# Optimization experiments

Hardware: AMD Instinct MI355X
Metric: run time of the kernel (lower is better)

The kernel has to match this reference:

```python
import jax, jax.numpy as jnp
import numpy as np

N = 100000   # nodes
E = 600000   # edges
D = 128      # in_dim == out_dim
ED = 6       # edge_dim
LN_EPS = 1e-5


def setup_inputs() -> dict:
    key = jax.random.key(0)
    ks = jax.random.split(key, 12)
    s = 1.0 / np.sqrt(D)
    se = 1.0 / np.sqrt(ED)
    return {
        "x": jax.random.normal(ks[0], (N, D), dtype=jnp.float32),
        "edge_index": jax.random.randint(ks[1], (2, E), 0, N, dtype=jnp.int64),
        "edge_attr": jax.random.normal(ks[2], (E, ED), dtype=jnp.float32),
        "batch": jnp.zeros((N,), dtype=jnp.int64),
        "W_e": jax.random.uniform(ks[3], (ED, D), jnp.float32, -se, se),
        "b_e": jax.random.uniform(ks[4], (D,), jnp.float32, -se, se),
        "eps": jnp.zeros((), dtype=jnp.float32),  # GINE train_eps init 0
        "W1": jax.random.uniform(ks[5], (D, D), jnp.float32, -s, s),
        "b1": jax.random.uniform(ks[6], (D,), jnp.float32, -s, s),
        "W2": jax.random.uniform(ks[7], (D, D), jnp.float32, -s, s),
        "b2": jax.random.uniform(ks[8], (D,), jnp.float32, -s, s),
        "gamma": jnp.ones((D,), dtype=jnp.float32),
        "beta": jnp.zeros((D,), dtype=jnp.float32),
    }


def reference(x, edge_index, edge_attr, batch, W_e, b_e, eps, W1, b1, W2, b2, gamma, beta):
    src, dst = edge_index[0], edge_index[1]
    # edge embedding: Linear(edge_dim -> in_dim)
    edge_emb = edge_attr @ W_e + b_e                      # [E, D]
    # GINEConv message: ReLU(x_j + edge_emb), scatter-add to target nodes
    msg = jax.nn.relu(x[src] + edge_emb)                  # [E, D]
    agg = jax.ops.segment_sum(msg, dst, num_segments=N)   # [N, D]
    h = (1.0 + eps) * x + agg                             # [N, D]
    # GINE nn: Linear -> ReLU -> Linear
    h = jax.nn.relu(h @ W1 + b1) @ W2 + b2                # [N, D]
    # LayerNorm over feature dim
    mu = jnp.mean(h, axis=-1, keepdims=True)
    var = jnp.var(h, axis=-1, keepdims=True)
    h = (h - mu) * jax.lax.rsqrt(var + LN_EPS) * gamma + beta
    # activation=True -> ReLU; dropout identity in eval mode
    return jax.nn.relu(h)
```

## Files before the change

### kernel.cpp

```cpp
#include <hip/hip_runtime.h>
#include <stdint.h>

#define NN 100000
#define EE 600000
#define DD 128

typedef _Float16 half8 __attribute__((ext_vector_type(8)));
typedef _Float16 h2 __attribute__((ext_vector_type(2)));
typedef float f32x4 __attribute__((ext_vector_type(4)));

static __device__ __forceinline__ uint32_t pack2(float a, float b) {
    h2 h; h.x = (_Float16)a; h.y = (_Float16)b;
    return __builtin_bit_cast(uint32_t, h);
}
static __device__ __forceinline__ h2 cvt22(float2 f) {
    h2 r; r.x = (_Float16)f.x; r.y = (_Float16)f.y; return r;
}
static __device__ __forceinline__ h2 bc_lo(h2 v) { h2 r; r.x = v.x; r.y = v.x; return r; }
static __device__ __forceinline__ h2 bc_hi(h2 v) { h2 r; r.x = v.y; r.y = v.y; return r; }

static __device__ __forceinline__ uint32_t edge_msg2(uint32_t rY, uint32_t rZ, uint32_t rW,
                                                     uint32_t xv, uint32_t bb,
                                                     uint32_t w0, uint32_t w1, uint32_t w2,
                                                     uint32_t w3, uint32_t w4, uint32_t w5)
{
    uint32_t m;
    asm("v_pk_fma_f16 %0, %1, %2, %3 op_sel:[0,0,0] op_sel_hi:[0,1,1]"
        : "=v"(m) : "v"(rY), "v"(w0), "v"(bb));
    asm("v_pk_fma_f16 %0, %1, %2, %0 op_sel:[1,0,0] op_sel_hi:[1,1,1]" : "+v"(m) : "v"(rY), "v"(w1));
    asm("v_pk_fma_f16 %0, %1, %2, %0 op_sel:[0,0,0] op_sel_hi:[0,1,1]" : "+v"(m) : "v"(rZ), "v"(w2));
    asm("v_pk_fma_f16 %0, %1, %2, %0 op_sel:[1,0,0] op_sel_hi:[1,1,1]" : "+v"(m) : "v"(rZ), "v"(w3));
    asm("v_pk_fma_f16 %0, %1, %2, %0 op_sel:[0,0,0] op_sel_hi:[0,1,1]" : "+v"(m) : "v"(rW), "v"(w4));
    asm("v_pk_fma_f16 %0, %1, %2, %0 op_sel:[1,0,0] op_sel_hi:[1,1,1]" : "+v"(m) : "v"(rW), "v"(w5));
    asm("v_pk_add_f16 %0, %0, %1" : "+v"(m) : "v"(xv));
    asm("v_pk_max_f16 %0, %0, 0" : "+v"(m));
    return m;
}

#define NB_HIST ((EE + 255) / 256)
#define NB_CONV (NN * DD / 4 / 256)
template<bool CONV>
__global__ __launch_bounds__(256)
void setup_kernel(const int* __restrict__ ei, const float* __restrict__ x,
                  const float* __restrict__ W1, const float* __restrict__ W2,
                  int* __restrict__ counts, uint32_t* __restrict__ xh,
                  _Float16* __restrict__ w1h, _Float16* __restrict__ w2h)
{
    const int nbc = CONV ? NB_CONV : 0;
    const int b = blockIdx.x, tid = threadIdx.x;
    if (b < NB_HIST) {
        int e = b * 256 + tid;
        if (e < EE) atomicAdd(&counts[ei[EE + e]], 1);
    } else if (CONV && b < NB_HIST + nbc) {
        int i = (b - NB_HIST) * 256 + tid;
        float4 v = ((const float4*)x)[i];
        uint2 o; o.x = pack2(v.x, v.y); o.y = pack2(v.z, v.w);
        ((uint2*)xh)[i] = o;
    } else {
        int t = (b - NB_HIST - nbc) * 256 + tid;
        if (t < 2 * DD * DD) {
            int which = t >> 14;
            int idx = t & (DD * DD - 1);
            int k = idx >> 7, d = idx & 127;
            float wv = (which ? W2 : W1)[k * DD + d];
            int kt = k >> 5, kr = k & 31;
            int grp = kr >> 3, j = kr & 7;
            int nt = d >> 4, cc = d & 15;
            int off = ((kt * 8 + nt) * 64 + grp * 16 + cc) * 8 + j;
            (which ? w2h : w1h)[off] = (_Float16)wv;
        }
    }
}

__global__ __launch_bounds__(256)
void scan_blocks(const int* __restrict__ counts, int* __restrict__ startv,
                 int* __restrict__ bsum)
{
    const int t = threadIdx.x;
    const int idx = blockIdx.x * 1024 + t * 4;
    int4 v = {0, 0, 0, 0};
    if (idx < NN) v = *(const int4*)(counts + idx);
    int s1 = v.x + v.y, s2 = s1 + v.z, s3 = s2 + v.w;
    const int lane = t & 63;
    int q = s3;
#pragma unroll
    for (int off = 1; off < 64; off <<= 1) {
        int u = __shfl_up(q, off, 64);
        if (lane >= off) q += u;
    }
    __shared__ int wsum[4];
    if (lane == 63) wsum[t >> 6] = q;
    __syncthreads();
    const int w = t >> 6;
    int pre = 0;
    if (w > 0) pre += wsum[0];
    if (w > 1) pre += wsum[1];
    if (w > 2) pre += wsum[2];
    const int excl = (q - s3) + pre;
    if (idx < NN) {
        int4 o = {excl, excl + v.x, excl + s1, excl + s2};
        *(int4*)(startv + idx) = o;
    }
    __syncthreads();
    if (t == 0) bsum[blockIdx.x] = wsum[0] + wsum[1] + wsum[2] + wsum[3];
}

__global__ __launch_bounds__(128)
void scan_top(const int* __restrict__ bsum, int* __restrict__ boff)
{
    __shared__ int sm[128];
    const int t = threadIdx.x;
    const int NB = (NN + 1023) / 1024;
    int v = (t < NB) ? bsum[t] : 0;
    sm[t] = v;
    __syncthreads();
#pragma unroll
    for (int off = 1; off < 128; off <<= 1) {
        int u = (t >= off) ? sm[t - off] : 0;
        __syncthreads();
        sm[t] += u;
        __syncthreads();
    }
    boff[t] = sm[t] - v;
}

__global__ __launch_bounds__(256)
void scatter_rec(const int* __restrict__ ei, const float* __restrict__ ea,
                 const int* __restrict__ start, const int* __restrict__ boff,
                 int* __restrict__ cursor, float* __restrict__ rec)
{
    int e = blockIdx.x * 256 + threadIdx.x;
    if (e >= EE) return;
    int dst = ei[EE + e];
    int src = ei[e];
    int pos = start[dst] + boff[dst >> 10] + atomicAdd(&cursor[dst], 1);
    const float2* eap = (const float2*)(ea + e * 6);
    float2 e01 = eap[0];
    float2 e23 = eap[1];
    float2 e45 = eap[2];
    float4 r;
    r.x = __int_as_float(src << 6);
    r.y = __uint_as_float(pack2(e01.x, e01.y));
    r.z = __uint_as_float(pack2(e23.x, e23.y));
    r.w = __uint_as_float(pack2(e45.x, e45.y));
    *(float4*)(rec + (size_t)pos * 4) = r;
}

__global__ __launch_bounds__(256, 4)
void fused_an(const uint32_t* __restrict__ xh, const float4* __restrict__ rec,
              const float* __restrict__ We, const float* __restrict__ be,
              const int* __restrict__ start, const int* __restrict__ boff,
              const float* __restrict__ epsp,
              const _Float16* __restrict__ w1h, const _Float16* __restrict__ w2h,
              const float* __restrict__ b1, const float* __restrict__ b2,
              const float* __restrict__ gamma, const float* __restrict__ beta,
              float* __restrict__ out)
{
    __shared__ _Float16 hbuf[4][16 * 128];
    const int wv = threadIdx.x >> 6;
    const int lane = threadIdx.x & 63;
    const int n0w = blockIdx.x * 64 + wv * 16;
    _Float16* hb = hbuf[wv];

    if (n0w < NN) {
        int n1w = n0w + 16; if (n1w > NN) n1w = NN;
        const int span = n1w - n0w;
        const int d0 = lane * 2;
        const uint32_t w0u = __builtin_bit_cast(uint32_t, cvt22(*(const float2*)(We + 0 * DD + d0)));
        const uint32_t w1u = __builtin_bit_cast(uint32_t, cvt22(*(const float2*)(We + 1 * DD + d0)));
        const uint32_t w2u = __builtin_bit_cast(uint32_t, cvt22(*(const float2*)(We + 2 * DD + d0)));
        const uint32_t w3u = __builtin_bit_cast(uint32_t, cvt22(*(const float2*)(We + 3 * DD + d0)));
        const uint32_t w4u = __builtin_bit_cast(uint32_t, cvt22(*(const float2*)(We + 4 * DD + d0)));
        const uint32_t w5u = __builtin_bit_cast(uint32_t, cvt22(*(const float2*)(We + 5 * DD + d0)));
        const uint32_t bbu = __builtin_bit_cast(uint32_t, cvt22(*(const float2*)(be + d0)));
        const float sc = 1.0f + epsp[0];

        int gs = 0;
        {
            int nidx = n0w + lane;
            if (lane <= span) gs = (nidx < NN) ? (start[nidx] + boff[nidx >> 10]) : EE;
        }
        const int ebase = __shfl(gs, 0, 64);
        const int eend  = __shfl(gs, span, 64);

        int n = n0w;
        int nstop = __shfl(gs, 1, 64);
        h2 xnh = __builtin_bit_cast(h2, xh[((uint32_t)n0w << 6) + lane]);
        float ax = 0.f, ay = 0.f;

#define LOAD_BATCH(EB, RARR, XARR)                                               \
        {                                                                        \
            const int last = eend - 1;                                           \
            _Pragma("unroll")                                                    \
            for (int k = 0; k < 8; ++k) {                                        \
                int ik = (EB) + k;                                               \
                RARR[k] = rec[ik < eend ? ik : last];                            \
            }                                                                    \
            _Pragma("unroll")                                                    \
            for (int k = 0; k < 8; ++k)                                          \
                XARR[k] = xh[(uint32_t)__float_as_int(RARR[k].x) + lane];        \
        }

#define FLUSH_H0()                                                               \
        {                                                                        \
            const int row = n - n0w;                                             \
            *(uint32_t*)&hb[row * 128 + (d0 ^ ((row & 7) << 4))] =               \
                pack2(fmaf(sc, (float)xnh.x, ax), fmaf(sc, (float)xnh.y, ay));   \
        }

#define STEP(K, MK)                                                              \
        {                                                                        \
            const int ek = e + K;                                                \
            if (ek < eend) {                                                     \
                while (ek >= nstop) {                                            \
                    FLUSH_H0();                                                  \
                    ax = 0.f; ay = 0.f; ++n;                                     \
                    xnh = __builtin_bit_cast(h2, xh[((uint32_t)n << 6) + lane]); \
                    nstop = __shfl(gs, n - n0w + 1, 64);                         \
                }                                                                \
                h2 mh = __builtin_bit_cast(h2, MK);                              \
                ax += (float)mh.x; ay += (float)mh.y;                            \
            }                                                                    \
        }

        float4 rc[8];
        uint32_t xc[8];
        if (ebase < eend) LOAD_BATCH(ebase, rc, xc);

        for (int e = ebase; e < eend; e += 8) {
            float4 rn[8];
            uint32_t xvn[8];
            const int en = e + 8;
            if (en < eend) {
                LOAD_BATCH(en, rn, xvn);
            } else {
#pragma unroll
                for (int k = 0; k < 8; ++k) { rn[k] = rc[k]; xvn[k] = xc[k]; }
            }
            uint32_t m[8];
#pragma unroll
            for (int k = 0; k < 8; ++k)
                m[k] = edge_msg2(__float_as_uint(rc[k].y), __float_as_uint(rc[k].z),
                                 __float_as_uint(rc[k].w), xc[k], bbu,
                                 w0u, w1u, w2u, w3u, w4u, w5u);
            STEP(0, m[0])
            STEP(1, m[1])
            STEP(2, m[2])
            STEP(3, m[3])
            STEP(4, m[4])
            STEP(5, m[5])
            STEP(6, m[6])
            STEP(7, m[7])
#pragma unroll
            for (int k = 0; k < 8; ++k) { rc[k] = rn[k]; xc[k] = xvn[k]; }
        }
#undef STEP
#undef LOAD_BATCH

        while (n < n1w) {
            FLUSH_H0();
            ax = 0.f; ay = 0.f; ++n;
            if (n < n1w) xnh = __builtin_bit_cast(h2, xh[((uint32_t)n << 6) + lane]);
        }
#undef FLUSH_H0
    }

    const int l  = lane;
    const int lm = l & 15;
    const int lg = l >> 4;
    const int r0 = n0w;

    half8 a1[4];
    {
        const int sw = (lm & 7) << 4;
        const _Float16* rowp = hb + lm * 128;
#pragma unroll
        for (int kt = 0; kt < 4; ++kt) {
            const int kb = kt * 32 + lg * 8;
            a1[kt] = *(const half8*)(rowp + (kb ^ sw));
        }
    }

    f32x4 acc[8];
#pragma unroll
    for (int nt = 0; nt < 8; ++nt) { acc[nt][0]=0.f; acc[nt][1]=0.f; acc[nt][2]=0.f; acc[nt][3]=0.f; }
#pragma unroll
    for (int kt = 0; kt < 4; ++kt) {
#pragma unroll
        for (int nt = 0; nt < 8; ++nt) {
            half8 bh = *(const half8*)(w1h + ((size_t)((kt * 8 + nt) * 64 + l)) * 8);
            acc[nt] = __builtin_amdgcn_mfma_f32_16x16x32_f16(a1[kt], bh, acc[nt], 0, 0, 0);
        }
    }

#pragma unroll
    for (int nt = 0; nt < 8; ++nt) {
        const int col = nt * 16 + lm;
        const float bias = b1[col];
#pragma unroll
        for (int q = 0; q < 4; ++q) {
            const int row = lg * 4 + q;
            float v1 = fmaxf(acc[nt][q] + bias, 0.f);
            hb[row * 128 + (col ^ ((row & 7) << 4))] = (_Float16)v1;
        }
    }

    half8 a2[4];
    {
        const int sw = (lm & 7) << 4;
        const _Float16* rowp = hb + lm * 128;
#pragma unroll
        for (int kt = 0; kt < 4; ++kt) {
            const int kb = kt * 32 + lg * 8;
            a2[kt] = *(const half8*)(rowp + (kb ^ sw));
        }
    }

    f32x4 acc2[8];
#pragma unroll
    for (int nt = 0; nt < 8; ++nt) { acc2[nt][0]=0.f; acc2[nt][1]=0.f; acc2[nt][2]=0.f; acc2[nt][3]=0.f; }
#pragma unroll
    for (int kt = 0; kt < 4; ++kt) {
#pragma unroll
        for (int nt = 0; nt < 8; ++nt) {
            half8 bh = *(const half8*)(w2h + ((size_t)((kt * 8 + nt) * 64 + l)) * 8);
            acc2[nt] = __builtin_amdgcn_mfma_f32_16x16x32_f16(a2[kt], bh, acc2[nt], 0, 0, 0);
        }
    }

    float sums[4] = {0,0,0,0}, sqs[4] = {0,0,0,0};
#pragma unroll
    for (int nt = 0; nt < 8; ++nt) {
        const float bias = b2[nt * 16 + lm];
#pragma unroll
        for (int q = 0; q < 4; ++q) {
            float v2 = acc2[nt][q] + bias;
            sums[q] += v2;
            sqs[q]  += v2 * v2;
        }
    }
#pragma unroll
    for (int m = 1; m < 16; m <<= 1) {
#pragma unroll
        for (int q = 0; q < 4; ++q) {
            sums[q] += __shfl_xor(sums[q], m, 64);
            sqs[q]  += __shfl_xor(sqs[q],  m, 64);
        }
    }

    float gam[8], bet[8], b2r[8];
#pragma unroll
    for (int nt = 0; nt < 8; ++nt) {
        gam[nt] = gamma[nt * 16 + lm];
        bet[nt] = beta[nt * 16 + lm];
        b2r[nt] = b2[nt * 16 + lm];
    }
#pragma unroll
    for (int q = 0; q < 4; ++q) {
        const int grow = r0 + lg * 4 + q;
        if (grow < NN) {
            const float mu  = sums[q] * (1.f / 128.f);
            const float var = sqs[q] * (1.f / 128.f) - mu * mu;
            const float rs  = rsqrtf(var + 1e-5f);
#pragma unroll
            for (int nt = 0; nt < 8; ++nt) {
                float v2 = acc2[nt][q] + b2r[nt];
                out[(size_t)grow * DD + nt * 16 + lm] =
                    fmaxf((v2 - mu) * rs * gam[nt] + bet[nt], 0.f);
            }
        }
    }
}

#define NWAVE 8192
__global__ __launch_bounds__(256)
void agg_pk(const float* __restrict__ x, const float* __restrict__ rec,
            const float* __restrict__ We, const float* __restrict__ be,
            const int* __restrict__ start, const int* __restrict__ boff,
            const int* __restrict__ counts, const float* __restrict__ epsp,
            uint32_t* __restrict__ h0h)
{
    const int w = blockIdx.x * 4 + (threadIdx.x >> 6);
    const int lane = threadIdx.x & 63;
    const int d0 = lane * 2;
    const h2 w0h = cvt22(*(const float2*)(We + 0 * DD + d0));
    const h2 w1h = cvt22(*(const float2*)(We + 1 * DD + d0));
    const h2 w2h = cvt22(*(const float2*)(We + 2 * DD + d0));
    const h2 w3h = cvt22(*(const float2*)(We + 3 * DD + d0));
    const h2 w4h = cvt22(*(const float2*)(We + 4 * DD + d0));
    const h2 w5h = cvt22(*(const float2*)(We + 5 * DD + d0));
    const h2 bbh = cvt22(*(const float2*)(be + d0));
    h2 zero2; zero2.x = (_Float16)0.f; zero2.y = (_Float16)0.f;
    const float sc = 1.0f + epsp[0];
    const int n0 = (int)(((long long)w * NN) >> 13);
    const int n1 = (int)(((long long)(w + 1) * NN) >> 13);

    for (int n = n0; n < n1; ++n) {
        const int begin = start[n] + boff[n >> 10];
        const int cnt = counts[n];
        const float4* rp = (const float4*)rec + begin;
        float ax = 0.f, ay = 0.f;
        for (int i = 0; i < cnt; ++i) {
            float4 r = rp[i];
            int s64 = __float_as_int(r.x);
            h2 c01 = __builtin_bit_cast(h2, r.y);
            h2 c23 = __builtin_bit_cast(h2, r.z);
            h2 c45 = __builtin_bit_cast(h2, r.w);
            h2 emb = bbh;
            emb = bc_lo(c01) * w0h + emb;
            emb = bc_hi(c01) * w1h + emb;
            emb = bc_lo(c23) * w2h + emb;
            emb = bc_hi(c23) * w3h + emb;
            emb = bc_lo(c45) * w4h + emb;
            emb = bc_hi(c45) * w5h + emb;
            h2 m = emb + cvt22(*(const float2*)(x + (size_t)s64 * 2 + d0));
            m = __builtin_elementwise_max(m, zero2);
            ax += (float)m.x;
            ay += (float)m.y;
        }
        float2 xn = *(const float2*)(x + (size_t)n * DD + d0);
        h0h[(size_t)n * 64 + lane] = pack2(fmaf(sc, xn.x, ax), fmaf(sc, xn.y, ay));
    }
}

__global__ __launch_bounds__(256)
void node_f16(const uint32_t* __restrict__ h0h,
              const _Float16* __restrict__ w1h, const _Float16* __restrict__ w2h,
              const float* __restrict__ b1, const float* __restrict__ b2,
              const float* __restrict__ gamma, const float* __restrict__ beta,
              float* __restrict__ out)
{
    __shared__ _Float16 h1buf[4][16 * 128];
    const int wv = threadIdx.x >> 6;
    const int l  = threadIdx.x & 63;
    const int lm = l & 15;
    const int lg = l >> 4;
    const int rbase = blockIdx.x * 128 + wv * 32;

    float gam[8], bet[8];
#pragma unroll
    for (int nt = 0; nt < 8; ++nt) {
        gam[nt] = gamma[nt * 16 + lm];
        bet[nt] = beta[nt * 16 + lm];
    }

    for (int t = 0; t < 2; ++t) {
        const int r0 = rbase + t * 16;
        int arow = r0 + lm;
        if (arow >= NN) arow = NN - 1;

        half8 a1[4];
#pragma unroll
        for (int kt = 0; kt < 4; ++kt) {
            const int kb = kt * 32 + lg * 8;
            a1[kt] = *(const half8*)((const _Float16*)h0h + (size_t)arow * DD + kb);
        }

        f32x4 acc[8];
#pragma unroll
        for (int nt = 0; nt < 8; ++nt) { acc[nt][0]=0.f; acc[nt][1]=0.f; acc[nt][2]=0.f; acc[nt][3]=0.f; }
#pragma unroll
        for (int kt = 0; kt < 4; ++kt) {
#pragma unroll
            for (int nt = 0; nt < 8; ++nt) {
                half8 bh = *(const half8*)(w1h + ((size_t)((kt * 8 + nt) * 64 + l)) * 8);
                acc[nt] = __builtin_amdgcn_mfma_f32_16x16x32_f16(a1[kt], bh, acc[nt], 0, 0, 0);
            }
        }

        _Float16* hb = h1buf[wv];
#pragma unroll
        for (int nt = 0; nt < 8; ++nt) {
            const int col = nt * 16 + lm;
            const float bias = b1[col];
#pragma unroll
            for (int q = 0; q < 4; ++q) {
                const int row = lg * 4 + q;
                float v1 = fmaxf(acc[nt][q] + bias, 0.f);
                hb[row * 128 + (col ^ ((row & 7) << 4))] = (_Float16)v1;
            }
        }

        half8 a2[4];
        {
            const int sw = (lm & 7) << 4;
            const _Float16* rowp = hb + lm * 128;
#pragma unroll
            for (int kt = 0; kt < 4; ++kt) {
                const int kb = kt * 32 + lg * 8;
                a2[kt] = *(const half8*)(rowp + (kb ^ sw));
            }
        }

        f32x4 acc2[8];
#pragma unroll
        for (int nt = 0; nt < 8; ++nt) { acc2[nt][0]=0.f; acc2[nt][1]=0.f; acc2[nt][2]=0.f; acc2[nt][3]=0.f; }
#pragma unroll
        for (int kt = 0; kt < 4; ++kt) {
#pragma unroll
            for (int nt = 0; nt < 8; ++nt) {
                half8 bh = *(const half8*)(w2h + ((size_t)((kt * 8 + nt) * 64 + l)) * 8);
                acc2[nt] = __builtin_amdgcn_mfma_f32_16x16x32_f16(a2[kt], bh, acc2[nt], 0, 0, 0);
            }
        }

        float vv[8][4];
        float sums[4] = {0,0,0,0}, sqs[4] = {0,0,0,0};
#pragma unroll
        for (int nt = 0; nt < 8; ++nt) {
            const int col = nt * 16 + lm;
            const float bias = b2[col];
#pragma unroll
            for (int q = 0; q < 4; ++q) {
                float v2 = acc2[nt][q] + bias;
                vv[nt][q] = v2;
                sums[q] += v2;
                sqs[q]  += v2 * v2;
            }
        }
#pragma unroll
        for (int m = 1; m < 16; m <<= 1) {
#pragma unroll
            for (int q = 0; q < 4; ++q) {
                sums[q] += __shfl_xor(sums[q], m, 64);
                sqs[q]  += __shfl_xor(sqs[q],  m, 64);
            }
        }
#pragma unroll
        for (int q = 0; q < 4; ++q) {
            const int grow = r0 + lg * 4 + q;
            if (grow < NN) {
                const float mu  = sums[q] * (1.f / 128.f);
                const float var = sqs[q] * (1.f / 128.f) - mu * mu;
                const float rs  = rsqrtf(var + 1e-5f);
#pragma unroll
                for (int nt = 0; nt < 8; ++nt) {
                    out[(size_t)grow * DD + nt * 16 + lm] =
                        fmaxf((vv[nt][q] - mu) * rs * gam[nt] + bet[nt], 0.f);
                }
            }
        }
    }
}

__global__ __launch_bounds__(256)
void prep_w(const float* __restrict__ W1, const float* __restrict__ W2,
            _Float16* __restrict__ w1h, _Float16* __restrict__ w2h)
{
    int t = blockIdx.x * 256 + threadIdx.x;
    if (t >= 2 * DD * DD) return;
    int which = t >> 14;
    int idx = t & (DD * DD - 1);
    int k = idx >> 7, d = idx & 127;
    float wv = (which ? W2 : W1)[k * DD + d];
    int kt = k >> 5, kr = k & 31;
    int grp = kr >> 3, j = kr & 7;
    int nt = d >> 4, cc = d & 15;
    int off = ((kt * 8 + nt) * 64 + grp * 16 + cc) * 8 + j;
    (which ? w2h : w1h)[off] = (_Float16)wv;
}

__global__ __launch_bounds__(256)
void edge_kernel(const float* __restrict__ x, const int* __restrict__ ei,
                 const float* __restrict__ ea, const float* __restrict__ We,
                 const float* __restrict__ be, float* agg)
{
    int tid = blockIdx.x * 256 + threadIdx.x;
    int d0 = (tid & 31) * 4;
    float4 w0 = *(const float4*)(We + 0 * DD + d0);
    float4 w1 = *(const float4*)(We + 1 * DD + d0);
    float4 w2 = *(const float4*)(We + 2 * DD + d0);
    float4 w3 = *(const float4*)(We + 3 * DD + d0);
    float4 w4 = *(const float4*)(We + 4 * DD + d0);
    float4 w5 = *(const float4*)(We + 5 * DD + d0);
    float4 bb = *(const float4*)(be + d0);
    int estride = (gridDim.x * 256) >> 5;
    for (int e = tid >> 5; e < EE; e += estride) {
        int src = ei[e];
        int dst = ei[EE + e];
        const float2* eap = (const float2*)(ea + e * 6);
        float2 e01 = eap[0];
        float2 e23 = eap[1];
        float2 e45 = eap[2];
        float4 xj = *(const float4*)(x + (size_t)src * DD + d0);
        float mx = xj.x + bb.x + e01.x*w0.x + e01.y*w1.x + e23.x*w2.x + e23.y*w3.x + e45.x*w4.x + e45.y*w5.x;
        float my = xj.y + bb.y + e01.x*w0.y + e01.y*w1.y + e23.x*w2.y + e23.y*w3.y + e45.x*w4.y + e45.y*w5.y;
        float mz = xj.z + bb.z + e01.x*w0.z + e01.y*w1.z + e23.x*w2.z + e23.y*w3.z + e45.x*w4.z + e45.y*w5.z;
        float mw = xj.w + bb.w + e01.x*w0.w + e01.y*w1.w + e23.x*w2.w + e23.y*w3.w + e45.x*w4.w + e45.y*w5.w;
        float* ap = agg + (size_t)dst * DD + d0;
        atomicAdd(ap + 0, fmaxf(mx, 0.f));
        atomicAdd(ap + 1, fmaxf(my, 0.f));
        atomicAdd(ap + 2, fmaxf(mz, 0.f));
        atomicAdd(ap + 3, fmaxf(mw, 0.f));
    }
}

__global__ __launch_bounds__(256)
void node2c(const float* __restrict__ aggp, const float* __restrict__ xp,
            const _Float16* __restrict__ w1h, const _Float16* __restrict__ w2h,
            const float* __restrict__ b1, const float* __restrict__ b2,
            const float* __restrict__ gamma, const float* __restrict__ beta,
            const float* __restrict__ epsp, float* __restrict__ out)
{
    __shared__ _Float16 h1buf[4][16 * 128];
    const int wv = threadIdx.x >> 6;
    const int l  = threadIdx.x & 63;
    const int lm = l & 15;
    const int lg = l >> 4;
    const int rbase = blockIdx.x * 128 + wv * 32;

    float gam[8], bet[8];
#pragma unroll
    for (int nt = 0; nt < 8; ++nt) {
        gam[nt] = gamma[nt * 16 + lm];
        bet[nt] = beta[nt * 16 + lm];
    }

    for (int t = 0; t < 2; ++t) {
        const int r0 = rbase + t * 16;
        int arow = r0 + lm;
        if (arow >= NN) arow = NN - 1;

        half8 a1[4];
#pragma unroll
        for (int kt = 0; kt < 4; ++kt) {
            const int kb = kt * 32 + lg * 8;
            const float4* hp = (const float4*)(aggp + (size_t)arow * DD + kb);
            float4 p0 = hp[0], p1 = hp[1];
            const float scale = 1.0f + epsp[0];
            const float4* xr = (const float4*)(xp + (size_t)arow * DD + kb);
            float4 x0 = xr[0], x1 = xr[1];
            float v[8] = { x0.x*scale+p0.x, x0.y*scale+p0.y, x0.z*scale+p0.z, x0.w*scale+p0.w,
                           x1.x*scale+p1.x, x1.y*scale+p1.y, x1.z*scale+p1.z, x1.w*scale+p1.w };
#pragma unroll
            for (int j = 0; j < 8; ++j) a1[kt][j] = (_Float16)v[j];
        }

        f32x4 acc[8];
#pragma unroll
        for (int nt = 0; nt < 8; ++nt) { acc[nt][0]=0.f; acc[nt][1]=0.f; acc[nt][2]=0.f; acc[nt][3]=0.f; }
#pragma unroll
        for (int kt = 0; kt < 4; ++kt) {
#pragma unroll
            for (int nt = 0; nt < 8; ++nt) {
                half8 bh = *(const half8*)(w1h + ((size_t)((kt * 8 + nt) * 64 + l)) * 8);
                acc[nt] = __builtin_amdgcn_mfma_f32_16x16x32_f16(a1[kt], bh, acc[nt], 0, 0, 0);
            }
        }

        _Float16* hb = h1buf[wv];
#pragma unroll
        for (int nt = 0; nt < 8; ++nt) {
            const int col = nt * 16 + lm;
            const float bias = b1[col];
#pragma unroll
            for (int q = 0; q < 4; ++q) {
                const int row = lg * 4 + q;
                float v1 = fmaxf(acc[nt][q] + bias, 0.f);
                hb[row * 128 + (col ^ ((row & 7) << 4))] = (_Float16)v1;
            }
        }

        half8 a2[4];
        {
            const int sw = (lm & 7) << 4;
            const _Float16* rowp = hb + lm * 128;
#pragma unroll
            for (int kt = 0; kt < 4; ++kt) {
                const int kb = kt * 32 + lg * 8;
                a2[kt] = *(const half8*)(rowp + (kb ^ sw));
            }
        }

        f32x4 acc2[8];
#pragma unroll
        for (int nt = 0; nt < 8; ++nt) { acc2[nt][0]=0.f; acc2[nt][1]=0.f; acc2[nt][2]=0.f; acc2[nt][3]=0.f; }
#pragma unroll
        for (int kt = 0; kt < 4; ++kt) {
#pragma unroll
            for (int nt = 0; nt < 8; ++nt) {
                half8 bh = *(const half8*)(w2h + ((size_t)((kt * 8 + nt) * 64 + l)) * 8);
                acc2[nt] = __builtin_amdgcn_mfma_f32_16x16x32_f16(a2[kt], bh, acc2[nt], 0, 0, 0);
            }
        }

        float vv[8][4];
        float sums[4] = {0,0,0,0}, sqs[4] = {0,0,0,0};
#pragma unroll
        for (int nt = 0; nt < 8; ++nt) {
            const int col = nt * 16 + lm;
            const float bias = b2[col];
#pragma unroll
            for (int q = 0; q < 4; ++q) {
                float v2 = acc2[nt][q] + bias;
                vv[nt][q] = v2;
                sums[q] += v2;
                sqs[q]  += v2 * v2;
            }
        }
#pragma unroll
        for (int m = 1; m < 16; m <<= 1) {
#pragma unroll
            for (int q = 0; q < 4; ++q) {
                sums[q] += __shfl_xor(sums[q], m, 64);
                sqs[q]  += __shfl_xor(sqs[q],  m, 64);
            }
        }
#pragma unroll
        for (int q = 0; q < 4; ++q) {
            const int grow = r0 + lg * 4 + q;
            if (grow < NN) {
                const float mu  = sums[q] * (1.f / 128.f);
                const float var = sqs[q] * (1.f / 128.f) - mu * mu;
                const float rs  = rsqrtf(var + 1e-5f);
#pragma unroll
                for (int nt = 0; nt < 8; ++nt) {
                    out[(size_t)grow * DD + nt * 16 + lm] =
                        fmaxf((vv[nt][q] - mu) * rs * gam[nt] + bet[nt], 0.f);
                }
            }
        }
    }
}

extern "C" void kernel_launch(void* const* d_in, const int* in_sizes, int n_in,
                              void* d_out, int out_size, void* d_ws, size_t ws_size,
                              hipStream_t stream) {
    (void)in_sizes; (void)n_in; (void)out_size;
    const float* x     = (const float*)d_in[0];
    const int*   ei    = (const int*)d_in[1];
    const float* ea    = (const float*)d_in[2];
    const float* We    = (const float*)d_in[4];
    const float* be    = (const float*)d_in[5];
    const float* epsp  = (const float*)d_in[6];
    const float* W1    = (const float*)d_in[7];
    const float* b1    = (const float*)d_in[8];
    const float* W2    = (const float*)d_in[9];
    const float* b2    = (const float*)d_in[10];
    const float* gamma = (const float*)d_in[11];
    const float* beta  = (const float*)d_in[12];
    float* out = (float*)d_out;

    char* ws = (char*)d_ws;
    _Float16* w1h = (_Float16*)ws;
    _Float16* w2h = w1h + DD * DD;
    size_t off = 2 * (size_t)DD * DD * sizeof(_Float16);
    int* counts = (int*)(ws + off);   off += (size_t)NN * 4;
    int* cursor = (int*)(ws + off);   off += (size_t)NN * 4;
    int* start  = (int*)(ws + off);   off += (size_t)NN * 4;
    int* bsum   = (int*)(ws + off);   off += 512;
    int* boff   = (int*)(ws + off);   off += 512;
    float* rec  = (float*)(ws + off); off += (size_t)EE * 16;
    uint32_t* h0h = (uint32_t*)(ws + off); off += (size_t)NN * DD * 2;
    const size_t need_h0 = off;
    uint32_t* xh  = (uint32_t*)(ws + off); off += (size_t)NN * DD * 2;
    const size_t need_xh = off;

    const int node_blocks = (NN + 127) / 128;
    const int fused_blocks = (NN + 63) / 64;
    const int NBLK = (NN + 1023) / 1024;

    if (ws_size >= need_h0) {
        const bool conv = (ws_size >= need_xh);
        hipMemsetAsync(counts, 0, 2 * (size_t)NN * 4, stream);
        if (conv) {
            setup_kernel<true><<<NB_HIST + NB_CONV + 128, 256, 0, stream>>>(
                ei, x, W1, W2, counts, xh, w1h, w2h);
        } else {
            setup_kernel<false><<<NB_HIST + 128, 256, 0, stream>>>(
                ei, x, W1, W2, counts, xh, w1h, w2h);
        }
        scan_blocks<<<NBLK, 256, 0, stream>>>(counts, start, bsum);
        scan_top<<<1, 128, 0, stream>>>(bsum, boff);
        scatter_rec<<<(EE + 255) / 256, 256, 0, stream>>>(ei, ea, start, boff, cursor, rec);
        if (conv) {
            fused_an<<<fused_blocks, 256, 0, stream>>>(xh, (const float4*)rec, We, be,
                                                       start, boff, epsp, w1h, w2h,
                                                       b1, b2, gamma, beta, out);
        } else {
            agg_pk<<<NWAVE / 4, 256, 0, stream>>>(x, rec, We, be, start, boff,
                                                  counts, epsp, h0h);
            node_f16<<<node_blocks, 256, 0, stream>>>(h0h, w1h, w2h, b1, b2, gamma, beta, out);
        }
    } else {
        hipMemsetAsync(d_out, 0, (size_t)NN * DD * sizeof(float), stream);
        prep_w<<<(2 * DD * DD + 255) / 256, 256, 0, stream>>>(W1, W2, w1h, w2h);
        edge_kernel<<<2048, 256, 0, stream>>>(x, ei, ea, We, be, out);
        node2c<<<node_blocks, 256, 0, stream>>>(out, x, w1h, w2h, b1, b2,
                                                gamma, beta, epsp, out);
    }
}
```

Measured before the change: 143.1 us.

## Split each node group's edge range across two waves and merge in LDS

Each 16-node group is now handled by a pair of waves instead of one. Each wave in the pair aggregates half of the group's CSR edge range into its own LDS tile, and only the first wave adds the self term. After a block barrier, the first wave sums the two fp16 partial tiles and runs the MLP and LayerNorm alone, while the second wave exits. The goal is more outstanding gather loads per node group in the latency-bound aggregation phase. The cost is twice as many blocks, an extra barrier, idle waves during the MLP, and an extra fp16 rounding when the partials are combined.

```diff
diff --git a/kernel.cpp b/kernel.cpp
--- a/kernel.cpp
+++ b/kernel.cpp
@@ -159,7 +159,9 @@
     __shared__ _Float16 hbuf[4][16 * 128];
     const int wv = threadIdx.x >> 6;
     const int lane = threadIdx.x & 63;
-    const int n0w = blockIdx.x * 64 + wv * 16;
+    const int pair = wv >> 1;
+    const int half = wv & 1;
+    const int n0w = blockIdx.x * 32 + pair * 16;
     _Float16* hb = hbuf[wv];
 
     if (n0w < NN) {
@@ -173,7 +175,7 @@
         const uint32_t w4u = __builtin_bit_cast(uint32_t, cvt22(*(const float2*)(We + 4 * DD + d0)));
         const uint32_t w5u = __builtin_bit_cast(uint32_t, cvt22(*(const float2*)(We + 5 * DD + d0)));
         const uint32_t bbu = __builtin_bit_cast(uint32_t, cvt22(*(const float2*)(be + d0)));
-        const float sc = 1.0f + epsp[0];
+        const float scw = half ? 0.f : (1.0f + epsp[0]);
 
         int gs = 0;
         {
@@ -182,6 +184,9 @@
         }
         const int ebase = __shfl(gs, 0, 64);
         const int eend  = __shfl(gs, span, 64);
+        const int emid  = (ebase + eend) >> 1;
+        const int myBase = half ? emid : ebase;
+        const int myEnd  = half ? eend : emid;
 
         int n = n0w;
         int nstop = __shfl(gs, 1, 64);
@@ -190,11 +195,11 @@
 
 #define LOAD_BATCH(EB, RARR, XARR)                                               \
         {                                                                        \
-            const int last = eend - 1;                                           \
+            const int last = myEnd - 1;                                          \
             _Pragma("unroll")                                                    \
             for (int k = 0; k < 8; ++k) {                                        \
                 int ik = (EB) + k;                                               \
-                RARR[k] = rec[ik < eend ? ik : last];                            \
+                RARR[k] = rec[ik < myEnd ? ik : last];                           \
             }                                                                    \
             _Pragma("unroll")                                                    \
             for (int k = 0; k < 8; ++k)                                          \
@@ -205,13 +210,13 @@
         {                                                                        \
             const int row = n - n0w;                                             \
             *(uint32_t*)&hb[row * 128 + (d0 ^ ((row & 7) << 4))] =               \
-                pack2(fmaf(sc, (float)xnh.x, ax), fmaf(sc, (float)xnh.y, ay));   \
+                pack2(fmaf(scw, (float)xnh.x, ax), fmaf(scw, (float)xnh.y, ay)); \
         }
 
 #define STEP(K, MK)                                                              \
         {                                                                        \
             const int ek = e + K;                                                \
-            if (ek < eend) {                                                     \
+            if (ek < myEnd) {                                                    \
                 while (ek >= nstop) {                                            \
                     FLUSH_H0();                                                  \
                     ax = 0.f; ay = 0.f; ++n;                                     \
@@ -225,13 +230,13 @@
 
         float4 rc[8];
         uint32_t xc[8];
-        if (ebase < eend) LOAD_BATCH(ebase, rc, xc);
-
-        for (int e = ebase; e < eend; e += 8) {
+        if (myBase < myEnd) LOAD_BATCH(myBase, rc, xc);
+
+        for (int e = myBase; e < myEnd; e += 8) {
             float4 rn[8];
             uint32_t xvn[8];
             const int en = e + 8;
-            if (en < eend) {
+            if (en < myEnd) {
                 LOAD_BATCH(en, rn, xvn);
             } else {
 #pragma unroll
@@ -265,6 +270,10 @@
 #undef FLUSH_H0
     }
 
+    __syncthreads();
+
+    if (half != 0 || n0w >= NN) return;
+
     const int l  = lane;
     const int lm = l & 15;
     const int lg = l >> 4;
@@ -273,13 +282,18 @@
     half8 a1[4];
     {
         const int sw = (lm & 7) << 4;
-        const _Float16* rowp = hb + lm * 128;
+        const _Float16* rowA = hbuf[wv] + lm * 128;
+        const _Float16* rowB = hbuf[wv + 1] + lm * 128;
 #pragma unroll
         for (int kt = 0; kt < 4; ++kt) {
             const int kb = kt * 32 + lg * 8;
-            a1[kt] = *(const half8*)(rowp + (kb ^ sw));
-        }
-    }
+            half8 va = *(const half8*)(rowA + (kb ^ sw));
+            half8 vb = *(const half8*)(rowB + (kb ^ sw));
+            a1[kt] = va + vb;
+        }
+    }
+
+    _Float16* hb0 = hbuf[wv];
 
     f32x4 acc[8];
 #pragma unroll
@@ -301,14 +315,14 @@
         for (int q = 0; q < 4; ++q) {
             const int row = lg * 4 + q;
             float v1 = fmaxf(acc[nt][q] + bias, 0.f);
-            hb[row * 128 + (col ^ ((row & 7) << 4))] = (_Float16)v1;
+            hb0[row * 128 + (col ^ ((row & 7) << 4))] = (_Float16)v1;
         }
     }
 
     half8 a2[4];
     {
         const int sw = (lm & 7) << 4;
-        const _Float16* rowp = hb + lm * 128;
+        const _Float16* rowp = hb0 + lm * 128;
 #pragma unroll
         for (int kt = 0; kt < 4; ++kt) {
             const int kb = kt * 32 + lg * 8;
@@ -757,7 +771,7 @@
     const size_t need_xh = off;
 
     const int node_blocks = (NN + 127) / 128;
-    const int fused_blocks = (NN + 63) / 64;
+    const int fused_blocks = (NN + 31) / 32;
     const int NBLK = (NN + 1023) / 1024;
 
     if (ws_size >= need_h0) {
```

Result: slower. 149.0 us (+4.1%).
